# Performance work log

Hardware: AMD Instinct MI355X
Metric: run time of the kernel (lower is better)

## Reference

```python
import jax, jax.numpy as jnp
import numpy as np

USER, ITEM, LATDIM, HYPER, FDIM, GL, LEAKY = 100000, 200000, 64, 128, 16, 2, 0.5
N = USER + ITEM
E = 3000000
LN_EPS = 1e-5


def _leaky(x):
    return jnp.where(x > 0, x, LEAKY * x)


def _ln(x, g, b):
    m = jnp.mean(x, axis=-1, keepdims=True)
    v = jnp.mean((x - m) ** 2, axis=-1, keepdims=True)
    return (x - m) * jax.lax.rsqrt(v + LN_EPS) * g + b


def _forward(fs, rows, cols):
    (uEmbeds, iEmbeds, uHyper, iHyper, u_attn, i_attn,
     dis_W1, dis_b1, dis_W2, dis_b2, dis_Wr1, dis_br1, dis_Wr2, dis_br2,
     dis_weights, dis_ln_g, dis_ln_b,
     gate_Wg1, gate_bg1, gate_Wg2, gate_bg2, gate_Wr1, gate_br1, gate_Wr2, gate_br2,
     gate_ln_g, gate_ln_b, adj_vals) = fs
    # Attention-weighted hyperedge incidence: softmax over the node axis (dim=0)
    uu = uEmbeds @ uHyper                       # [user, hyperNum]
    uu = uu * jax.nn.softmax(uu @ u_attn, axis=0)
    ii = iEmbeds @ iHyper                       # [item, hyperNum]
    ii = ii * jax.nn.softmax(ii @ i_attn, axis=0)
    x = jnp.concatenate([uEmbeds, iEmbeds], axis=0)  # [N, latdim]
    total = x
    for i in range(GL):
        # sparse GCN: spmm(adj, x) with COO edges (keepRate == 1 -> no edge drop)
        tem = jax.ops.segment_sum(adj_vals[:, None] * x[cols], rows, num_segments=N)
        # hypergraph conv: adj @ (adj.T @ x)
        hyp = jnp.concatenate([uu @ (uu.T @ x[:USER]), ii @ (ii.T @ x[USER:])], axis=0)

        def dis(z, j):
            # 4 disentanglers, batched over k via einsum
            h = _leaky(jnp.einsum('nd,kde->kne', z, dis_W1[i, j]) + dis_b1[i, j][:, None, :])
            f = jnp.einsum('kne,kef->knf', h, dis_W2[i, j]) + dis_b2[i, j][:, None, :]  # [4,N,fdim]
            comb = jnp.einsum('k,knf->nf', jax.nn.softmax(dis_weights[i, j]), f)
            rec = _leaky(comb @ dis_Wr1[i, j] + dis_br1[i, j]) @ dis_Wr2[i, j] + dis_br2[i, j]
            return _ln(z + rec, dis_ln_g[i, j], dis_ln_b[i, j])

        def gate(cur, prev):
            c = jnp.concatenate([cur, prev], axis=-1)  # [N, 2*latdim]
            gw = jax.nn.sigmoid(jax.nn.relu(c @ gate_Wg1[i] + gate_bg1[i]) @ gate_Wg2[i] + gate_bg2[i])
            res = _leaky(c @ gate_Wr1[i] + gate_br1[i]) @ gate_Wr2[i] + gate_br2[i]
            return _ln(gw * res + cur, gate_ln_g[i], gate_ln_b[i])

        x = gate(dis(tem, 0), x) + gate(dis(hyp, 1), x)
        total = total + x
    return total  # sum(lats): final node embeddings [N, latdim]


def setup_inputs() -> dict:
    key = jax.random.key(0)
    ks = iter(jax.random.split(key, 40))

    def rn(shape, scale=0.1):
        return jax.random.normal(next(ks), shape, dtype=jnp.float32) * scale

    return dict(
        uEmbeds=rn((USER, LATDIM)),
        iEmbeds=rn((ITEM, LATDIM)),
        uHyper=rn((LATDIM, HYPER)),
        iHyper=rn((LATDIM, HYPER)),
        u_attn=rn((HYPER, 1), 1.0),
        i_attn=rn((HYPER, 1), 1.0),
        dis_W1=rn((GL, 2, 4, LATDIM, LATDIM)),
        dis_b1=jnp.zeros((GL, 2, 4, LATDIM), jnp.float32),
        dis_W2=rn((GL, 2, 4, LATDIM, FDIM)),
        dis_b2=jnp.zeros((GL, 2, 4, FDIM), jnp.float32),
        dis_Wr1=rn((GL, 2, FDIM, LATDIM)),
        dis_br1=jnp.zeros((GL, 2, LATDIM), jnp.float32),
        dis_Wr2=rn((GL, 2, LATDIM, LATDIM)),
        dis_br2=jnp.zeros((GL, 2, LATDIM), jnp.float32),
        dis_weights=jnp.ones((GL, 2, 4), jnp.float32) / 4.0,
        dis_ln_g=jnp.ones((GL, 2, LATDIM), jnp.float32),
        dis_ln_b=jnp.zeros((GL, 2, LATDIM), jnp.float32),
        gate_Wg1=rn((GL, 2 * LATDIM, LATDIM)),
        gate_bg1=jnp.zeros((GL, LATDIM), jnp.float32),
        gate_Wg2=rn((GL, LATDIM, LATDIM)),
        gate_bg2=jnp.zeros((GL, LATDIM), jnp.float32),
        gate_Wr1=rn((GL, 2 * LATDIM, LATDIM)),
        gate_br1=jnp.zeros((GL, LATDIM), jnp.float32),
        gate_Wr2=rn((GL, LATDIM, LATDIM)),
        gate_br2=jnp.zeros((GL, LATDIM), jnp.float32),
        gate_ln_g=jnp.ones((GL, LATDIM), jnp.float32),
        gate_ln_b=jnp.zeros((GL, LATDIM), jnp.float32),
        adj_vals=jax.random.uniform(next(ks), (E,), dtype=jnp.float32) * 0.1,
        adj_rows=jax.random.randint(next(ks), (E,), 0, N, dtype=jnp.int32),
        adj_cols=jax.random.randint(next(ks), (E,), 0, N, dtype=jnp.int32),
        keep_rate=1,
    )


def reference(uEmbeds, iEmbeds, uHyper, iHyper, u_attn, i_attn,
              dis_W1, dis_b1, dis_W2, dis_b2, dis_Wr1, dis_br1, dis_Wr2, dis_br2,
              dis_weights, dis_ln_g, dis_ln_b,
              gate_Wg1, gate_bg1, gate_Wg2, gate_bg2, gate_Wr1, gate_br1, gate_Wr2, gate_br2,
              gate_ln_g, gate_ln_b, adj_vals, adj_rows, adj_cols, keep_rate):
    fs = (uEmbeds, iEmbeds, uHyper, iHyper, u_attn, i_attn,
          dis_W1, dis_b1, dis_W2, dis_b2, dis_Wr1, dis_br1, dis_Wr2, dis_br2,
          dis_weights, dis_ln_g, dis_ln_b,
          gate_Wg1, gate_bg1, gate_Wg2, gate_bg2, gate_Wr1, gate_br1, gate_Wr2, gate_br2,
          gate_ln_g, gate_ln_b, adj_vals)
    return _forward(fs, adj_rows, adj_cols)
```

## Files before the change

### kernel.cpp

```cpp
#include <hip/hip_runtime.h>
#include <math.h>

#define USERN 100000
#define ITEMN 200000
#define NND   300000
#define DD    64
#define HH    128
#define FF    16
#define EDG   3000000
#define LEAKY_A 0.5f
#define LN_EPS  1e-5f
#define SCHUNK 1024
#define SNB ((NND+SCHUNK-1)/SCHUNK)
#define PROWS (NND/8)

typedef __attribute__((ext_vector_type(8))) short bf16x8;
typedef __attribute__((ext_vector_type(4))) float f32x4;
#define MFMA16(a,b,c) __builtin_amdgcn_mfma_f32_16x16x32_bf16(a,b,c,0,0,0)

__device__ __forceinline__ float leaky(float x){ return x>0.f ? x : LEAKY_A*x; }
__device__ __forceinline__ unsigned fenc(float f){ unsigned u=__float_as_uint(f); return (u&0x80000000u)? ~u : (u|0x80000000u); }
__device__ __forceinline__ float fdec(unsigned u){ return (u&0x80000000u)? __uint_as_float(u&0x7fffffffu) : __uint_as_float(~u); }
__device__ __forceinline__ short f2bf(float f){
  unsigned u=__float_as_uint(f);
  unsigned r=u + 0x7fffu + ((u>>16)&1u);
  return (short)(r>>16);
}
__device__ __forceinline__ float bf2f(short s){
  return __uint_as_float(((unsigned)(unsigned short)s)<<16);
}
__device__ __forceinline__ bf16x8 loadAbf(const short* __restrict__ base, int l, int dbase){
  const short* p = base + (size_t)(l&15)*DD + dbase + ((l>>4)<<2);
  int2 a=*(const int2*)p;
  int2 b=*(const int2*)(p+16);
  bf16x8 r;
  ((int2*)&r)[0]=a; ((int2*)&r)[1]=b;
  return r;
}

__global__ __launch_bounds__(256) void k_init(const float* __restrict__ uE, const float* __restrict__ iE,
                        short* __restrict__ x, float* __restrict__ out){
  int tot=NND*DD;
  for(int idx=blockIdx.x*256+threadIdx.x; idx<tot; idx+=gridDim.x*256){
    int n=idx>>6;
    float v=(n<USERN)? uE[idx] : iE[idx-USERN*DD];
    x[idx]=f2bf(v); out[idx]=v;
  }
}

__global__ __launch_bounds__(128) void k_hv(const float* __restrict__ uH,const float* __restrict__ iH,
      const float* __restrict__ uA,const float* __restrict__ iA,float* __restrict__ hv){
  int t=threadIdx.x;
  const float* H=(t<64)? uH:iH;
  const float* A=(t<64)? uA:iA;
  int d=t&63;
  float s=0.f;
  for(int h=0;h<HH;h++) s=fmaf(H[d*HH+h],A[h],s);
  hv[t]=s;
}

__global__ __launch_bounds__(256) void k_att(const float* __restrict__ E, const float* __restrict__ hvp,
      float* __restrict__ a, int U){
  __shared__ float hs[64];
  int tid=threadIdx.x;
  if(tid<64) hs[tid]=hvp[tid];
  __syncthreads();
  int wave=tid>>6, lane=tid&63;
  for(int g=blockIdx.x*4+wave; g<U/4; g+=gridDim.x*4){
    int n0=g*4;
    #pragma unroll
    for(int m=0;m<4;m++){
      float p=E[(size_t)(n0+m)*DD+lane]*hs[lane];
      #pragma unroll
      for(int off=32;off;off>>=1) p+=__shfl_xor(p,off,64);
      if(lane==0) a[n0+m]=p;
    }
  }
}

__global__ __launch_bounds__(256) void k_redmax(const float* __restrict__ a, int n, unsigned* slot){
  float v=-3.0e38f;
  for(int i=blockIdx.x*256+threadIdx.x;i<n;i+=gridDim.x*256) v=fmaxf(v,a[i]);
  #pragma unroll
  for(int off=32;off;off>>=1) v=fmaxf(v,__shfl_xor(v,off,64));
  if((threadIdx.x&63)==0) atomicMax(slot, fenc(v));
}

__global__ __launch_bounds__(256) void k_sumexp(const float* __restrict__ a, int n,
      const unsigned* __restrict__ mslot, float* ssum){
  float mx=fdec(*mslot);
  float s=0.f;
  for(int i=blockIdx.x*256+threadIdx.x;i<n;i+=gridDim.x*256) s+=expf(a[i]-mx);
  #pragma unroll
  for(int off=32;off;off>>=1) s+=__shfl_xor(s,off,64);
  if((threadIdx.x&63)==0) atomicAdd(ssum, s);
}

__global__ __launch_bounds__(256) void k_scale_a(float* __restrict__ a,int n,
      const unsigned* __restrict__ mslot,const float* __restrict__ ssum){
  float mx=fdec(*mslot); float inv=1.f/(*ssum);
  for(int i=blockIdx.x*256+threadIdx.x;i<n;i+=gridDim.x*256) a[i]=expf(a[i]-mx)*inv;
}

__global__ __launch_bounds__(256) void k_hist8(const int* __restrict__ rows, int* __restrict__ cnt){
  int part=blockIdx.x&7;
  int bip=blockIdx.x>>3, nbp=gridDim.x>>3;
  int lo=part*PROWS, hi=lo+PROWS;
  for(int e=bip*256+threadIdx.x; e<EDG; e+=nbp*256){
    int r=rows[e];
    if(r>=lo && r<hi) atomicAdd(&cnt[r],1);
  }
}

__global__ __launch_bounds__(256) void k_scanA(int* __restrict__ cnt, int* __restrict__ bsum){
  __shared__ int part[256];
  int b=blockIdx.x, t=threadIdx.x;
  int base=b*SCHUNK;
  int v[4]; int s=0;
  #pragma unroll
  for(int k2=0;k2<4;k2++){
    int idx=base+t*4+k2;
    int val=(idx<NND)? cnt[idx]:0;
    v[k2]=s; s+=val;
  }
  part[t]=s;
  __syncthreads();
  for(int off=1;off<256;off<<=1){
    int y=(t>=off)? part[t-off]:0;
    __syncthreads();
    part[t]+=y;
    __syncthreads();
  }
  int excl=(t==0)?0:part[t-1];
  #pragma unroll
  for(int k2=0;k2<4;k2++){
    int idx=base+t*4+k2;
    if(idx<NND) cnt[idx]=excl+v[k2];
  }
  if(t==255) bsum[b]=part[255];
}

__global__ __launch_bounds__(512) void k_scanB(int* __restrict__ bsum){
  __shared__ int part[512];
  int t=threadIdx.x;
  part[t]=(t<SNB)? bsum[t]:0;
  __syncthreads();
  for(int off=1;off<512;off<<=1){
    int y=(t>=off)? part[t-off]:0;
    __syncthreads();
    part[t]+=y;
    __syncthreads();
  }
  if(t<SNB) bsum[t]=(t==0)?0:part[t-1];
}

__global__ __launch_bounds__(256) void k_scanC(int* __restrict__ rowptr, const int* __restrict__ bsum,
      int* __restrict__ wcur){
  for(int i=blockIdx.x*256+threadIdx.x; i<NND; i+=gridDim.x*256){
    int v=rowptr[i]+bsum[i>>10];
    rowptr[i]=v; wcur[i]=v;
  }
  if(blockIdx.x==0 && threadIdx.x==0) rowptr[NND]=EDG;
}

__global__ __launch_bounds__(256) void k_scatter8(const int* __restrict__ rows,const int* __restrict__ cols,
      const float* __restrict__ vals, int* __restrict__ wcur, int2* __restrict__ epack){
  int part=blockIdx.x&7;
  int bip=blockIdx.x>>3, nbp=gridDim.x>>3;
  int lo=part*PROWS, hi=lo+PROWS;
  for(int e=bip*256+threadIdx.x; e<EDG; e+=nbp*256){
    int r=rows[e];
    if(r>=lo && r<hi){
      int pos=atomicAdd(&wcur[r],1);
      epack[pos]=make_int2(cols[e], __float_as_int(vals[e]));
    }
  }
}

__global__ __launch_bounds__(512) void k_spmm_csr(const int* __restrict__ rowptr,
      const int2* __restrict__ epack,
      const short* __restrict__ x, short* __restrict__ tem){
  int wave=threadIdx.x>>6, lane=threadIdx.x&63;
  for(int r=blockIdx.x*8+wave; r<NND; r+=gridDim.x*8){
    int st=rowptr[r], en=rowptr[r+1];
    float acc=0.f;
    int p=st;
    for(; p+1<en; p+=2){
      int2 e0=epack[p], e1=epack[p+1];
      float x0=bf2f(x[(size_t)e0.x*DD+lane]);
      float x1=bf2f(x[(size_t)e1.x*DD+lane]);
      acc=fmaf(__int_as_float(e0.y),x0,acc);
      acc=fmaf(__int_as_float(e1.y),x1,acc);
    }
    if(p<en){ int2 e0=epack[p]; acc=fmaf(__int_as_float(e0.y), bf2f(x[(size_t)e0.x*DD+lane]), acc); }
    tem[(size_t)r*DD+lane]=f2bf(acc);
  }
}

__global__ __launch_bounds__(256) void k_gacc(const float* __restrict__ E,const float* __restrict__ sca,
      const short* __restrict__ x,float* __restrict__ G,int U){
  __shared__ __align__(16) float es[4][256];
  int tid=threadIdx.x, wave=tid>>6, lane=tid&63;
  float acc[64];
  #pragma unroll
  for(int j=0;j<64;j++) acc[j]=0.f;
  float* esw=es[wave];
  for(int g=blockIdx.x*4+wave; g<U/4; g+=gridDim.x*4){
    int n0=g*4;
    float xv[4];
    #pragma unroll
    for(int m=0;m<4;m++){
      float sc=sca[n0+m];
      esw[m*64+lane]=E[(size_t)(n0+m)*DD+lane]*sc;
      xv[m]=bf2f(x[(size_t)(n0+m)*DD+lane]);
    }
    #pragma unroll
    for(int d4=0;d4<16;d4++){
      float4 eb[4];
      #pragma unroll
      for(int m=0;m<4;m++) eb[m]=((const float4*)(esw+m*64))[d4];
      #pragma unroll
      for(int c=0;c<4;c++){
        #pragma unroll
        for(int m=0;m<4;m++) acc[d4*4+c]=fmaf(((const float*)&eb[m])[c],xv[m],acc[d4*4+c]);
      }
    }
  }
  #pragma unroll
  for(int j=0;j<64;j++) atomicAdd(&G[j*64+lane],acc[j]);
}

__global__ __launch_bounds__(256) void k_tm(const float* __restrict__ uH,const float* __restrict__ iH,
      const float* __restrict__ G,float* __restrict__ Mo){
  __shared__ __align__(16) float Hs[64*HH];
  __shared__ __align__(16) float Gs[64*64];
  __shared__ __align__(16) float Ts[HH*64];
  const float* H = blockIdx.x ? iH : uH;
  const float* Gp = G + blockIdx.x*4096;
  float* Mp = Mo + blockIdx.x*4096;
  int tid=threadIdx.x;
  for(int k=tid;k<64*HH;k+=256) Hs[k]=H[k];
  for(int k=tid;k<4096;k+=256) Gs[k]=Gp[k];
  __syncthreads();
  int lane=tid&63, wq=tid>>6;
  float tac[32];
  #pragma unroll
  for(int k=0;k<32;k++) tac[k]=0.f;
  for(int d1=0;d1<64;d1++){
    float gv=Gs[d1*64+lane];
    const float4* hrow=(const float4*)(Hs+d1*HH+wq*32);
    #pragma unroll
    for(int k4=0;k4<8;k4++){
      float4 hb=hrow[k4];
      tac[k4*4+0]=fmaf(hb.x,gv,tac[k4*4+0]);
      tac[k4*4+1]=fmaf(hb.y,gv,tac[k4*4+1]);
      tac[k4*4+2]=fmaf(hb.z,gv,tac[k4*4+2]);
      tac[k4*4+3]=fmaf(hb.w,gv,tac[k4*4+3]);
    }
  }
  #pragma unroll
  for(int k=0;k<32;k++) Ts[(wq*32+k)*64+lane]=tac[k];
  __syncthreads();
  float mac[16];
  #pragma unroll
  for(int k=0;k<16;k++) mac[k]=0.f;
  for(int h=0;h<HH;h++){
    float tv=Ts[h*64+lane];
    #pragma unroll
    for(int k=0;k<16;k++) mac[k]=fmaf(Hs[(wq*16+k)*HH+h],tv,mac[k]);
  }
  #pragma unroll
  for(int k=0;k<16;k++) Mp[(wq*16+k)*64+lane]=mac[k];
}

__global__ __launch_bounds__(256) void k_hyp2(const float* __restrict__ E,const float* __restrict__ sca,
      const float* __restrict__ Mp,short* __restrict__ hyp,int U){
  __shared__ __align__(16) float es[4][256];
  int tid=threadIdx.x, wave=tid>>6, lane=tid&63;
  float mcol[64];
  #pragma unroll
  for(int j=0;j<64;j++) mcol[j]=Mp[j*64+lane];
  float* esw=es[wave];
  for(int g=blockIdx.x*4+wave; g<U/4; g+=gridDim.x*4){
    int n0=g*4;
    #pragma unroll
    for(int m=0;m<4;m++){
      float sc=sca[n0+m];
      esw[m*64+lane]=E[(size_t)(n0+m)*DD+lane]*sc;
    }
    float acc[4]={0,0,0,0};
    #pragma unroll
    for(int d4=0;d4<16;d4++){
      float4 eb[4];
      #pragma unroll
      for(int m=0;m<4;m++) eb[m]=((const float4*)(esw+m*64))[d4];
      #pragma unroll
      for(int c=0;c<4;c++){
        float mv=mcol[d4*4+c];
        #pragma unroll
        for(int m=0;m<4;m++) acc[m]=fmaf(((const float*)&eb[m])[c],mv,acc[m]);
      }
    }
    #pragma unroll
    for(int m=0;m<4;m++) hyp[(size_t)(n0+m)*DD+lane]=f2bf(acc[m]);
  }
}

__global__ __launch_bounds__(512) void k_dis2(
    short* __restrict__ tem, short* __restrict__ hyp,
    const float* __restrict__ W1b,const float* __restrict__ b1b,
    const float* __restrict__ W2b,const float* __restrict__ b2b,
    const float* __restrict__ Wr1b,const float* __restrict__ br1b,
    const float* __restrict__ Wr2b,const float* __restrict__ br2b,
    const float* __restrict__ wsoftb,const float* __restrict__ lngb,const float* __restrict__ lnbb,
    int layer){
  __shared__ __align__(16) short w1s[16384];
  __shared__ __align__(16) short w2s[4096];
  __shared__ __align__(16) short wr1s[2048];
  __shared__ __align__(16) short wr2s[4096];
  __shared__ __align__(16) short hst[8][1024];
  __shared__ __align__(16) short cst[8][512];
  __shared__ float swsh[4];
  int half=gridDim.x>>1;
  int sel=(blockIdx.x>=half);
  int bid=blockIdx.x - (sel? half:0);
  int ij=layer*2+sel;
  short* z = sel? hyp : tem;
  const float* W1 = W1b + (size_t)ij*4*64*64;
  const float* b1 = b1b + (size_t)ij*4*64;
  const float* W2 = W2b + (size_t)ij*4*64*16;
  const float* b2 = b2b + (size_t)ij*4*16;
  const float* Wr1= Wr1b+ (size_t)ij*16*64;
  const float* br1= br1b+ (size_t)ij*64;
  const float* Wr2= Wr2b+ (size_t)ij*64*64;
  const float* br2= br2b+ (size_t)ij*64;
  const float* wsoft=wsoftb+(size_t)ij*4;
  const float* lng= lngb + (size_t)ij*64;
  const float* lnb= lnbb + (size_t)ij*64;
  int tid=threadIdx.x;
  for(int t=tid;t<16384;t+=512){
    int j=t&7,kg=(t>>3)&3,c=(t>>5)&15,ot=(t>>9)&3,kb=(t>>11)&1,kk=t>>12;
    int k=kb*32+kg*4+(j&3)+((j>>2)<<4), o=ot*16+c;
    w1s[t]=f2bf(W1[(size_t)(kk*64+k)*64+o]);
  }
  for(int t=tid;t<4096;t+=512){
    int j=t&7,kg=(t>>3)&3,c=(t>>5)&15,kb=(t>>9)&1,kk=t>>10;
    int k=kb*32+kg*4+(j&3)+((j>>2)<<4);
    w2s[t]=f2bf(W2[(size_t)(kk*64+k)*16+c]);
  }
  for(int t=tid;t<2048;t+=512){
    int j=t&7,kg=(t>>3)&3,c=(t>>5)&15,ot=t>>9;
    int o=ot*16+c;
    short v=0;
    if(j<4){ int k=kg*4+j; v=f2bf(Wr1[k*64+o]); }
    wr1s[t]=v;
  }
  for(int t=tid;t<4096;t+=512){
    int j=t&7,kg=(t>>3)&3,c=(t>>5)&15,ot=(t>>9)&3,kb=t>>11;
    int k=kb*32+kg*4+(j&3)+((j>>2)<<4), o=ot*16+c;
    wr2s[t]=f2bf(Wr2[k*64+o]);
  }
  if(tid==0){
    float m0=fmaxf(fmaxf(wsoft[0],wsoft[1]),fmaxf(wsoft[2],wsoft[3]));
    float e0=expf(wsoft[0]-m0),e1=expf(wsoft[1]-m0),e2=expf(wsoft[2]-m0),e3=expf(wsoft[3]-m0);
    float s=e0+e1+e2+e3;
    swsh[0]=e0/s; swsh[1]=e1/s; swsh[2]=e2/s; swsh[3]=e3/s;
  }
  __syncthreads();
  int wave=tid>>6, l=tid&63, lr=l&15, lg=l>>4;
  float sw[4]; sw[0]=swsh[0]; sw[1]=swsh[1]; sw[2]=swsh[2]; sw[3]=swsh[3];
  float b1v[4][4], br1v[4], br2v[4], gv[4], bv[4];
  #pragma unroll
  for(int kk=0;kk<4;kk++)
    #pragma unroll
    for(int ot=0;ot<4;ot++) b1v[kk][ot]=b1[kk*64+ot*16+lr];
  float b2c = sw[0]*b2[lr] + sw[1]*b2[16+lr] + sw[2]*b2[32+lr] + sw[3]*b2[48+lr];
  #pragma unroll
  for(int ot=0;ot<4;ot++){
    br1v[ot]=br1[ot*16+lr]; br2v[ot]=br2[ot*16+lr];
    gv[ot]=lng[ot*16+lr];   bv[ot]=lnb[ot*16+lr];
  }
  short* hw=hst[wave];
  short* cw=cst[wave];
  for(int t=l;t<256;t+=64){
    int r=t>>4, lgp=(t>>2)&3, jj=t&3;
    cw[(r*4+lgp)*8+4+jj]=0;
  }
  int slot=(lr*4+lg)*8;
  const f32x4 zero={0.f,0.f,0.f,0.f};
  for(int tile=bid*8+wave; tile<NND/16; tile+=half*8){
    int n0=tile*16;
    short* zrow=z+(size_t)n0*DD;
    bf16x8 A0=loadAbf(zrow,l,0), A1=loadAbf(zrow,l,32);
    f32x4 cba; cba[0]=b2c; cba[1]=b2c; cba[2]=b2c; cba[3]=b2c;
    #pragma unroll
    for(int kk=0;kk<4;kk++){
      const short* w1k=&w1s[kk*4096];
      #pragma unroll
      for(int ot=0;ot<4;ot++){
        f32x4 ha=zero;
        ha=MFMA16(A0,*(const bf16x8*)&w1k[ot*512+slot],ha);
        ha=MFMA16(A1,*(const bf16x8*)&w1k[2048+ot*512+slot],ha);
        int kb2=ot>>1;
        #pragma unroll
        for(int j=0;j<4;j++){
          int addr=kb2*512 + ((lg*4+j)*4 + (lr>>2))*8 + ((ot&1)<<2) + (l&3);
          hw[addr]=f2bf(leaky(ha[j]+b1v[kk][ot]));
        }
      }
      bf16x8 hA0=*(const bf16x8*)&hw[slot];
      bf16x8 hA1=*(const bf16x8*)&hw[512+slot];
      f32x4 fa=zero;
      fa=MFMA16(hA0,*(const bf16x8*)&w2s[kk*1024+slot],fa);
      fa=MFMA16(hA1,*(const bf16x8*)&w2s[kk*1024+512+slot],fa);
      float swk=sw[kk];
      #pragma unroll
      for(int j=0;j<4;j++) cba[j]=fmaf(swk,fa[j],cba[j]);
    }
    #pragma unroll
    for(int j=0;j<4;j++)
      cw[((lg*4+j)*4 + (lr>>2))*8 + (lr&3)] = f2bf(cba[j]);
    bf16x8 cA=*(const bf16x8*)&cw[slot];
    #pragma unroll
    for(int ot=0;ot<4;ot++){
      f32x4 ra=MFMA16(cA,*(const bf16x8*)&wr1s[ot*512+slot],zero);
      int kb2=ot>>1;
      #pragma unroll
      for(int j=0;j<4;j++){
        int addr=kb2*512 + ((lg*4+j)*4 + (lr>>2))*8 + ((ot&1)<<2) + (l&3);
        hw[addr]=f2bf(leaky(ra[j]+br1v[ot]));
      }
    }
    bf16x8 rA0=*(const bf16x8*)&hw[slot];
    bf16x8 rA1=*(const bf16x8*)&hw[512+slot];
    float y[4][4];
    #pragma unroll
    for(int ot=0;ot<4;ot++){
      f32x4 rc=zero;
      rc=MFMA16(rA0,*(const bf16x8*)&wr2s[ot*512+slot],rc);
      rc=MFMA16(rA1,*(const bf16x8*)&wr2s[2048+ot*512+slot],rc);
      #pragma unroll
      for(int j=0;j<4;j++){
        float zd=bf2f(zrow[(size_t)(lg*4+j)*DD + ot*16+lr]);
        y[ot][j]=zd + rc[j] + br2v[ot];
      }
    }
    #pragma unroll
    for(int j=0;j<4;j++){
      float s=y[0][j]+y[1][j]+y[2][j]+y[3][j];
      s+=__shfl_xor(s,1,64); s+=__shfl_xor(s,2,64); s+=__shfl_xor(s,4,64); s+=__shfl_xor(s,8,64);
      float mean=s*(1.f/64.f);
      float t0=y[0][j]-mean, t1=y[1][j]-mean, t2=y[2][j]-mean, t3=y[3][j]-mean;
      float s2=t0*t0+t1*t1+t2*t2+t3*t3;
      s2+=__shfl_xor(s2,1,64); s2+=__shfl_xor(s2,2,64); s2+=__shfl_xor(s2,4,64); s2+=__shfl_xor(s2,8,64);
      float inv=rsqrtf(s2*(1.f/64.f)+LN_EPS);
      zrow[(size_t)(lg*4+j)*DD +  0+lr]=f2bf(t0*inv*gv[0]+bv[0]);
      zrow[(size_t)(lg*4+j)*DD + 16+lr]=f2bf(t1*inv*gv[1]+bv[1]);
      zrow[(size_t)(lg*4+j)*DD + 32+lr]=f2bf(t2*inv*gv[2]+bv[2]);
      zrow[(size_t)(lg*4+j)*DD + 48+lr]=f2bf(t3*inv*gv[3]+bv[3]);
    }
  }
}

__global__ __launch_bounds__(512) void k_gate2(
    const short* __restrict__ tem, const short* __restrict__ hyp,
    short* __restrict__ x, float* __restrict__ out,
    const float* __restrict__ Wg1,const float* __restrict__ bg1,
    const float* __restrict__ Wg2,const float* __restrict__ bg2,
    const float* __restrict__ Wr1,const float* __restrict__ br1,
    const float* __restrict__ Wr2,const float* __restrict__ br2,
    const float* __restrict__ lng,const float* __restrict__ lnb){
  __shared__ __align__(16) short g1s[4*4*512];
  __shared__ __align__(16) short r1s[4*4*512];
  __shared__ __align__(16) short g2s[2*4*512];
  __shared__ __align__(16) short r2s[2*4*512];
  __shared__ __align__(16) short hls[8][2][1024];
  int tid=threadIdx.x;
  for(int t=tid;t<8192;t+=512){
    int j=t&7,kg=(t>>3)&3,c=(t>>5)&15,ot=(t>>9)&3,kb=t>>11;
    int k=kb*32+kg*4+(j&3)+((j>>2)<<4), o=ot*16+c;
    g1s[t]=f2bf(Wg1[k*64+o]);
    r1s[t]=f2bf(Wr1[k*64+o]);
  }
  for(int t=tid;t<4096;t+=512){
    int j=t&7,kg=(t>>3)&3,c=(t>>5)&15,ot=(t>>9)&3,kb=t>>11;
    int k=kb*32+kg*4+(j&3)+((j>>2)<<4), o=ot*16+c;
    g2s[t]=f2bf(Wg2[k*64+o]);
    r2s[t]=f2bf(Wr2[k*64+o]);
  }
  __syncthreads();
  int wave=tid>>6, l=tid&63;
  int lr=l&15, lg=l>>4;
  float bg1v[4],br1v[4],bg2v[4],br2v[4],gv[4],bv[4];
  #pragma unroll
  for(int ot=0;ot<4;ot++){
    bg1v[ot]=bg1[ot*16+lr]; br1v[ot]=br1[ot*16+lr];
    bg2v[ot]=bg2[ot*16+lr]; br2v[ot]=br2[ot*16+lr];
    gv[ot]=lng[ot*16+lr];   bv[ot]=lnb[ot*16+lr];
  }
  short* hG=&hls[wave][0][0];
  short* hR=&hls[wave][1][0];
  int slot=(lr*4+lg)*8;
  const f32x4 zero={0.f,0.f,0.f,0.f};
  for(int tile=blockIdx.x*8+wave; tile<NND/16; tile+=gridDim.x*8){
    int n0=tile*16;
    const short* xrow=x+(size_t)n0*DD;
    bf16x8 pA0=loadAbf(xrow,l,0), pA1=loadAbf(xrow,l,32);
    f32x4 pg[4],pr[4];
    #pragma unroll
    for(int ot=0;ot<4;ot++){
      f32x4 ag=zero, ar=zero;
      ag=MFMA16(pA0,*(const bf16x8*)&g1s[(2*4+ot)*512+slot],ag);
      ag=MFMA16(pA1,*(const bf16x8*)&g1s[(3*4+ot)*512+slot],ag);
      ar=MFMA16(pA0,*(const bf16x8*)&r1s[(2*4+ot)*512+slot],ar);
      ar=MFMA16(pA1,*(const bf16x8*)&r1s[(3*4+ot)*512+slot],ar);
      pg[ot]=ag; pr[ot]=ar;
    }
    float ya[4][4];
    #pragma unroll
    for(int p=0;p<2;p++){
      const short* cur=(p? hyp : tem)+(size_t)n0*DD;
      bf16x8 cA0=loadAbf(cur,l,0), cA1=loadAbf(cur,l,32);
      #pragma unroll
      for(int ot=0;ot<4;ot++){
        f32x4 ag=pg[ot], ar=pr[ot];
        ag=MFMA16(cA0,*(const bf16x8*)&g1s[(0*4+ot)*512+slot],ag);
        ag=MFMA16(cA1,*(const bf16x8*)&g1s[(1*4+ot)*512+slot],ag);
        ar=MFMA16(cA0,*(const bf16x8*)&r1s[(0*4+ot)*512+slot],ar);
        ar=MFMA16(cA1,*(const bf16x8*)&r1s[(1*4+ot)*512+slot],ar);
        int kb2=ot>>1;
        #pragma unroll
        for(int j=0;j<4;j++){
          int addr=kb2*512 + ((lg*4+j)*4 + (lr>>2))*8 + ((ot&1)<<2) + (l&3);
          hG[addr]=f2bf(fmaxf(ag[j]+bg1v[ot],0.f));
          hR[addr]=f2bf(leaky(ar[j]+br1v[ot]));
        }
      }
      bf16x8 hgA0=*(const bf16x8*)&hG[slot],    hgA1=*(const bf16x8*)&hG[512+slot];
      bf16x8 hrA0=*(const bf16x8*)&hR[slot],    hrA1=*(const bf16x8*)&hR[512+slot];
      f32x4 g2a[4], r2a[4];
      #pragma unroll
      for(int ot=0;ot<4;ot++){
        f32x4 ag=zero, ar=zero;
        ag=MFMA16(hgA0,*(const bf16x8*)&g2s[(0*4+ot)*512+slot],ag);
        ag=MFMA16(hgA1,*(const bf16x8*)&g2s[(1*4+ot)*512+slot],ag);
        ar=MFMA16(hrA0,*(const bf16x8*)&r2s[(0*4+ot)*512+slot],ar);
        ar=MFMA16(hrA1,*(const bf16x8*)&r2s[(1*4+ot)*512+slot],ar);
        g2a[ot]=ag; r2a[ot]=ar;
      }
      float y[4][4];
      #pragma unroll
      for(int ot=0;ot<4;ot++){
        #pragma unroll
        for(int j=0;j<4;j++){
          float cd=bf2f(cur[(size_t)(lg*4+j)*DD + ot*16+lr]);
          float gw=1.f/(1.f+expf(-(g2a[ot][j]+bg2v[ot])));
          y[ot][j]=gw*(r2a[ot][j]+br2v[ot])+cd;
        }
      }
      #pragma unroll
      for(int j=0;j<4;j++){
        float s=y[0][j]+y[1][j]+y[2][j]+y[3][j];
        s+=__shfl_xor(s,1,64); s+=__shfl_xor(s,2,64); s+=__shfl_xor(s,4,64); s+=__shfl_xor(s,8,64);
        float mean=s*(1.f/64.f);
        float t0=y[0][j]-mean, t1=y[1][j]-mean, t2=y[2][j]-mean, t3=y[3][j]-mean;
        float s2=t0*t0+t1*t1+t2*t2+t3*t3;
        s2+=__shfl_xor(s2,1,64); s2+=__shfl_xor(s2,2,64); s2+=__shfl_xor(s2,4,64); s2+=__shfl_xor(s2,8,64);
        float inv=rsqrtf(s2*(1.f/64.f)+LN_EPS);
        float yn0=t0*inv*gv[0]+bv[0];
        float yn1=t1*inv*gv[1]+bv[1];
        float yn2=t2*inv*gv[2]+bv[2];
        float yn3=t3*inv*gv[3]+bv[3];
        if(p==0){ ya[0][j]=yn0; ya[1][j]=yn1; ya[2][j]=yn2; ya[3][j]=yn3; }
        else    { ya[0][j]+=yn0; ya[1][j]+=yn1; ya[2][j]+=yn2; ya[3][j]+=yn3; }
      }
    }
    #pragma unroll
    for(int ot=0;ot<4;ot++){
      #pragma unroll
      for(int j=0;j<4;j++){
        size_t idx=(size_t)(n0+lg*4+j)*DD + ot*16+lr;
        x[idx]=f2bf(ya[ot][j]);
        out[idx]+=ya[ot][j];
      }
    }
  }
}

extern "C" void kernel_launch(void* const* d_in, const int* in_sizes, int n_in,
                              void* d_out, int out_size, void* d_ws, size_t ws_size,
                              hipStream_t stream){
  const float* uE  =(const float*)d_in[0];
  const float* iE  =(const float*)d_in[1];
  const float* uH  =(const float*)d_in[2];
  const float* iH  =(const float*)d_in[3];
  const float* uA  =(const float*)d_in[4];
  const float* iA  =(const float*)d_in[5];
  const float* dW1 =(const float*)d_in[6];
  const float* db1 =(const float*)d_in[7];
  const float* dW2 =(const float*)d_in[8];
  const float* db2 =(const float*)d_in[9];
  const float* dWr1=(const float*)d_in[10];
  const float* dbr1=(const float*)d_in[11];
  const float* dWr2=(const float*)d_in[12];
  const float* dbr2=(const float*)d_in[13];
  const float* dwts=(const float*)d_in[14];
  const float* dlng=(const float*)d_in[15];
  const float* dlnb=(const float*)d_in[16];
  const float* gWg1=(const float*)d_in[17];
  const float* gbg1=(const float*)d_in[18];
  const float* gWg2=(const float*)d_in[19];
  const float* gbg2=(const float*)d_in[20];
  const float* gWr1=(const float*)d_in[21];
  const float* gbr1=(const float*)d_in[22];
  const float* gWr2=(const float*)d_in[23];
  const float* gbr2=(const float*)d_in[24];
  const float* glng=(const float*)d_in[25];
  const float* glnb=(const float*)d_in[26];
  const float* avals=(const float*)d_in[27];
  const int*   arows=(const int*)d_in[28];
  const int*   acols=(const int*)d_in[29];
  float* out=(float*)d_out;

  size_t bfShorts = (size_t)3*NND*DD;
  size_t f32Floats = (size_t)NND + 128 + 8192 + 8192 + 8;
  size_t csrFloats = (size_t)2*EDG + (NND+1) + NND + 512;
  size_t needBase = bfShorts*sizeof(short) + f32Floats*sizeof(float);
  size_t needFull = needBase + csrFloats*sizeof(float);
  if(ws_size < needBase) return;
  bool persist = (ws_size >= needFull);

  short* x   = (short*)d_ws;
  short* tem = x   + (size_t)NND*DD;
  short* hyp = tem + (size_t)NND*DD;
  float* a   = (float*)(hyp + (size_t)NND*DD);
  float* hv  = a   + NND;
  float* G   = hv  + 128;
  float* Mb  = G   + 8192;
  float* red = Mb  + 8192;

  float* csrbase = persist ? (red + 8) : (float*)hyp;
  int2*  epack = (int2*)csrbase;
  int*   rowptr= (int*)(csrbase + 2*(size_t)EDG);
  int*   wcur  = rowptr + (NND+1);
  int*   bsum  = wcur + NND;

  hipMemsetAsync(red, 0, 8*sizeof(float), stream);
  k_init<<<2048,256,0,stream>>>(uE,iE,x,out);
  k_hv<<<1,128,0,stream>>>(uH,iH,uA,iA,hv);
  k_att<<<256,256,0,stream>>>(uE,hv,a,USERN);
  k_att<<<256,256,0,stream>>>(iE,hv+64,a+USERN,ITEMN);
  k_redmax<<<256,256,0,stream>>>(a,USERN,(unsigned*)red);
  k_redmax<<<256,256,0,stream>>>(a+USERN,ITEMN,(unsigned*)red+2);
  k_sumexp<<<256,256,0,stream>>>(a,USERN,(const unsigned*)red,red+1);
  k_sumexp<<<256,256,0,stream>>>(a+USERN,ITEMN,(const unsigned*)red+2,red+3);
  k_scale_a<<<256,256,0,stream>>>(a,USERN,(const unsigned*)red,red+1);
  k_scale_a<<<256,256,0,stream>>>(a+USERN,ITEMN,(const unsigned*)red+2,red+3);

  if(persist){
    hipMemsetAsync(rowptr,0,(NND+1)*sizeof(int),stream);
    k_hist8<<<2048,256,0,stream>>>(arows,rowptr);
    k_scanA<<<SNB,256,0,stream>>>(rowptr,bsum);
    k_scanB<<<1,512,0,stream>>>(bsum);
    k_scanC<<<2048,256,0,stream>>>(rowptr,bsum,wcur);
    k_scatter8<<<2048,256,0,stream>>>(arows,acols,avals,wcur,epack);
  }

  for(int i=0;i<2;i++){
    if(!persist){
      hipMemsetAsync(rowptr,0,(NND+1)*sizeof(int),stream);
      k_hist8<<<2048,256,0,stream>>>(arows,rowptr);
      k_scanA<<<SNB,256,0,stream>>>(rowptr,bsum);
      k_scanB<<<1,512,0,stream>>>(bsum);
      k_scanC<<<2048,256,0,stream>>>(rowptr,bsum,wcur);
      k_scatter8<<<2048,256,0,stream>>>(arows,acols,avals,wcur,epack);
    }
    k_spmm_csr<<<4096,512,0,stream>>>(rowptr,epack,x,tem);

    hipMemsetAsync(G,0,8192*sizeof(float),stream);
    k_gacc<<<256,256,0,stream>>>(uE,a,x,G,USERN);
    k_gacc<<<256,256,0,stream>>>(iE,a+USERN,x+(size_t)USERN*DD,G+4096,ITEMN);
    k_tm<<<2,256,0,stream>>>(uH,iH,G,Mb);
    k_hyp2<<<256,256,0,stream>>>(uE,a,Mb,hyp,USERN);
    k_hyp2<<<256,256,0,stream>>>(iE,a+USERN,Mb+4096,hyp+(size_t)USERN*DD,ITEMN);
    k_dis2<<<1024,512,0,stream>>>(tem,hyp,
      dW1,db1,dW2,db2,dWr1,dbr1,dWr2,dbr2,dwts,dlng,dlnb,i);
    k_gate2<<<512,512,0,stream>>>(tem,hyp,x,out,
      gWg1+(size_t)i*128*64, gbg1+(size_t)i*64,
      gWg2+(size_t)i*64*64,  gbg2+(size_t)i*64,
      gWr1+(size_t)i*128*64, gbr1+(size_t)i*64,
      gWr2+(size_t)i*64*64,  gbr2+(size_t)i*64,
      glng+(size_t)i*64, glnb+(size_t)i*64);
  }
}
```

Measured before the change: 2.076 ms.

## Ping-pong x buffers, defer fp32 output sum, and vectorize SpMM gathers

```diff
diff --git a/kernel.cpp b/kernel.cpp
--- a/kernel.cpp
+++ b/kernel.cpp
@@ -39,12 +39,20 @@
 }
 
 __global__ __launch_bounds__(256) void k_init(const float* __restrict__ uE, const float* __restrict__ iE,
-                        short* __restrict__ x, float* __restrict__ out){
+                        short* __restrict__ x){
   int tot=NND*DD;
   for(int idx=blockIdx.x*256+threadIdx.x; idx<tot; idx+=gridDim.x*256){
-    int n=idx>>6;
-    float v=(n<USERN)? uE[idx] : iE[idx-USERN*DD];
-    x[idx]=f2bf(v); out[idx]=v;
+    float v=(idx<USERN*DD)? uE[idx] : iE[idx-USERN*DD];
+    x[idx]=f2bf(v);
+  }
+}
+
+__global__ __launch_bounds__(256) void k_fin(const float* __restrict__ uE, const float* __restrict__ iE,
+      const short* __restrict__ x1, const short* __restrict__ x2, float* __restrict__ out){
+  int tot=NND*DD;
+  for(int idx=blockIdx.x*256+threadIdx.x; idx<tot; idx+=gridDim.x*256){
+    float v=(idx<USERN*DD)? uE[idx] : iE[idx-USERN*DD];
+    out[idx]=v + bf2f(x1[idx]) + bf2f(x2[idx]);
   }
 }
 
@@ -180,20 +188,30 @@
 __global__ __launch_bounds__(512) void k_spmm_csr(const int* __restrict__ rowptr,
       const int2* __restrict__ epack,
       const short* __restrict__ x, short* __restrict__ tem){
-  int wave=threadIdx.x>>6, lane=threadIdx.x&63;
-  for(int r=blockIdx.x*8+wave; r<NND; r+=gridDim.x*8){
+  int wave=threadIdx.x>>6, hw=(threadIdx.x>>5)&1, ln=threadIdx.x&31;
+  for(int r=blockIdx.x*16+wave*2+hw; r<NND; r+=gridDim.x*16){
     int st=rowptr[r], en=rowptr[r+1];
-    float acc=0.f;
+    float a0=0.f, a1=0.f;
     int p=st;
     for(; p+1<en; p+=2){
       int2 e0=epack[p], e1=epack[p+1];
-      float x0=bf2f(x[(size_t)e0.x*DD+lane]);
-      float x1=bf2f(x[(size_t)e1.x*DD+lane]);
-      acc=fmaf(__int_as_float(e0.y),x0,acc);
-      acc=fmaf(__int_as_float(e1.y),x1,acc);
-    }
-    if(p<en){ int2 e0=epack[p]; acc=fmaf(__int_as_float(e0.y), bf2f(x[(size_t)e0.x*DD+lane]), acc); }
-    tem[(size_t)r*DD+lane]=f2bf(acc);
+      int w0=*(const int*)(x+(size_t)e0.x*DD+ln*2);
+      int w1=*(const int*)(x+(size_t)e1.x*DD+ln*2);
+      float v0=__int_as_float(e0.y), v1=__int_as_float(e1.y);
+      a0=fmaf(v0, bf2f((short)(w0&0xffff)), a0);
+      a1=fmaf(v0, bf2f((short)(w0>>16)),    a1);
+      a0=fmaf(v1, bf2f((short)(w1&0xffff)), a0);
+      a1=fmaf(v1, bf2f((short)(w1>>16)),    a1);
+    }
+    if(p<en){
+      int2 e0=epack[p];
+      int w0=*(const int*)(x+(size_t)e0.x*DD+ln*2);
+      float v0=__int_as_float(e0.y);
+      a0=fmaf(v0, bf2f((short)(w0&0xffff)), a0);
+      a1=fmaf(v0, bf2f((short)(w0>>16)),    a1);
+    }
+    int outw = ((int)(unsigned short)f2bf(a0)) | (((int)f2bf(a1))<<16);
+    *(int*)(tem+(size_t)r*DD+ln*2) = outw;
   }
 }
 
@@ -464,7 +482,7 @@
 
 __global__ __launch_bounds__(512) void k_gate2(
     const short* __restrict__ tem, const short* __restrict__ hyp,
-    short* __restrict__ x, float* __restrict__ out,
+    const short* __restrict__ xin, short* __restrict__ xout,
     const float* __restrict__ Wg1,const float* __restrict__ bg1,
     const float* __restrict__ Wg2,const float* __restrict__ bg2,
     const float* __restrict__ Wr1,const float* __restrict__ br1,
@@ -504,7 +522,7 @@
   const f32x4 zero={0.f,0.f,0.f,0.f};
   for(int tile=blockIdx.x*8+wave; tile<NND/16; tile+=gridDim.x*8){
     int n0=tile*16;
-    const short* xrow=x+(size_t)n0*DD;
+    const short* xrow=xin+(size_t)n0*DD;
     bf16x8 pA0=loadAbf(xrow,l,0), pA1=loadAbf(xrow,l,32);
     f32x4 pg[4],pr[4];
     #pragma unroll
@@ -580,8 +598,7 @@
       #pragma unroll
       for(int j=0;j<4;j++){
         size_t idx=(size_t)(n0+lg*4+j)*DD + ot*16+lr;
-        x[idx]=f2bf(ya[ot][j]);
-        out[idx]+=ya[ot][j];
+        xout[idx]=f2bf(ya[ot][j]);
       }
     }
   }
@@ -622,7 +639,7 @@
   const int*   acols=(const int*)d_in[29];
   float* out=(float*)d_out;
 
-  size_t bfShorts = (size_t)3*NND*DD;
+  size_t bfShorts = (size_t)4*NND*DD;
   size_t f32Floats = (size_t)NND + 128 + 8192 + 8192 + 8;
   size_t csrFloats = (size_t)2*EDG + (NND+1) + NND + 512;
   size_t needBase = bfShorts*sizeof(short) + f32Floats*sizeof(float);
@@ -630,8 +647,9 @@
   if(ws_size < needBase) return;
   bool persist = (ws_size >= needFull);
 
-  short* x   = (short*)d_ws;
-  short* tem = x   + (size_t)NND*DD;
+  short* xA  = (short*)d_ws;
+  short* xB  = xA  + (size_t)NND*DD;
+  short* tem = xB  + (size_t)NND*DD;
   short* hyp = tem + (size_t)NND*DD;
   float* a   = (float*)(hyp + (size_t)NND*DD);
   float* hv  = a   + NND;
@@ -646,7 +664,7 @@
   int*   bsum  = wcur + NND;
 
   hipMemsetAsync(red, 0, 8*sizeof(float), stream);
-  k_init<<<2048,256,0,stream>>>(uE,iE,x,out);
+  k_init<<<2048,256,0,stream>>>(uE,iE,xA);
   k_hv<<<1,128,0,stream>>>(uH,iH,uA,iA,hv);
   k_att<<<256,256,0,stream>>>(uE,hv,a,USERN);
   k_att<<<256,256,0,stream>>>(iE,hv+64,a+USERN,ITEMN);
@@ -667,6 +685,8 @@
   }
 
   for(int i=0;i<2;i++){
+    short* xin = (i==0)? xA : xB;
+    short* xout= (i==0)? xB : xA;
     if(!persist){
       hipMemsetAsync(rowptr,0,(NND+1)*sizeof(int),stream);
       k_hist8<<<2048,256,0,stream>>>(arows,rowptr);
@@ -675,21 +695,22 @@
       k_scanC<<<2048,256,0,stream>>>(rowptr,bsum,wcur);
       k_scatter8<<<2048,256,0,stream>>>(arows,acols,avals,wcur,epack);
     }
-    k_spmm_csr<<<4096,512,0,stream>>>(rowptr,epack,x,tem);
+    k_spmm_csr<<<4096,512,0,stream>>>(rowptr,epack,xin,tem);
 
     hipMemsetAsync(G,0,8192*sizeof(float),stream);
-    k_gacc<<<256,256,0,stream>>>(uE,a,x,G,USERN);
-    k_gacc<<<256,256,0,stream>>>(iE,a+USERN,x+(size_t)USERN*DD,G+4096,ITEMN);
+    k_gacc<<<256,256,0,stream>>>(uE,a,xin,G,USERN);
+    k_gacc<<<256,256,0,stream>>>(iE,a+USERN,xin+(size_t)USERN*DD,G+4096,ITEMN);
     k_tm<<<2,256,0,stream>>>(uH,iH,G,Mb);
     k_hyp2<<<256,256,0,stream>>>(uE,a,Mb,hyp,USERN);
     k_hyp2<<<256,256,0,stream>>>(iE,a+USERN,Mb+4096,hyp+(size_t)USERN*DD,ITEMN);
     k_dis2<<<1024,512,0,stream>>>(tem,hyp,
       dW1,db1,dW2,db2,dWr1,dbr1,dWr2,dbr2,dwts,dlng,dlnb,i);
-    k_gate2<<<512,512,0,stream>>>(tem,hyp,x,out,
+    k_gate2<<<512,512,0,stream>>>(tem,hyp,xin,xout,
       gWg1+(size_t)i*128*64, gbg1+(size_t)i*64,
       gWg2+(size_t)i*64*64,  gbg2+(size_t)i*64,
       gWr1+(size_t)i*128*64, gbr1+(size_t)i*64,
       gWr2+(size_t)i*64*64,  gbr2+(size_t)i*64,
       glng+(size_t)i*64, glnb+(size_t)i*64);
   }
-}
+  k_fin<<<2048,256,0,stream>>>(uE,iE,xB,xA,out);
+}
```

Measured after the change: 1.820 ms. 1.14x faster.
